# Optimization experiments

Measured on AMD Instinct MI355X. Metric: run time of the kernel, lower is better.

Reference implementation:

```python
import jax, jax.numpy as jnp
import numpy as np

N, E, F, H, EF, ED, L, NL, NH, OD = 2048, 65536, 128, 512, 16, 64, 5, 4, 8, 64
MAX_DEG = 64


def _ln(x, s, b):
    m = x.mean(-1, keepdims=True)
    v = x.var(-1, keepdims=True)
    return (x - m) * jax.lax.rsqrt(v + 1e-5) * s + b


def setup_inputs() -> dict:
    key = jax.random.key(0)
    ks = jax.random.split(key, 40)
    s = 0.02
    x = jax.random.normal(ks[0], (N, F), jnp.float32)
    edge_index = jax.random.randint(ks[1], (2, E), 0, N, jnp.int32)
    edge_attr = jax.random.normal(ks[2], (E, EF), jnp.float32)
    # variable-length shortest paths, padded with -1
    plen = jax.random.randint(ks[3], (N, N), 0, L + 1, jnp.int32)
    pos = jnp.arange(L, dtype=jnp.int32)
    valid = pos[None, None, :] < plen[:, :, None]
    node_paths = jnp.where(valid, jax.random.randint(ks[4], (N, N, L), 0, N, jnp.int32), -1)
    edge_paths = jnp.where(valid, jax.random.randint(ks[5], (N, N, L), 0, E, jnp.int32), -1)
    p = {
        'x': x, 'edge_index': edge_index, 'edge_attr': edge_attr,
        'node_paths': node_paths, 'edge_paths': edge_paths,
        'W_node': s * jax.random.normal(ks[6], (F, H)), 'b_node': jnp.zeros((H,)),
        'W_edge': s * jax.random.normal(ks[7], (EF, ED)), 'b_edge': jnp.zeros((ED,)),
        'z_in': s * jax.random.normal(ks[8], (MAX_DEG, H)),
        'z_out': s * jax.random.normal(ks[9], (MAX_DEG, H)),
        'b_spatial': s * jax.random.normal(ks[10], (L,)),
        'edge_vector': s * jax.random.normal(ks[11], (L, ED)),
        'ln1_s': jnp.ones((NL, H)), 'ln1_b': jnp.zeros((NL, H)),
        'Wq': s * jax.random.normal(ks[12], (NL, H, H)), 'bq': jnp.zeros((NL, H)),
        'Wk': s * jax.random.normal(ks[13], (NL, H, H)), 'bk': jnp.zeros((NL, H)),
        'Wv': s * jax.random.normal(ks[14], (NL, H, H)), 'bv': jnp.zeros((NL, H)),
        'Wo': s * jax.random.normal(ks[15], (NL, H, H)), 'bo': jnp.zeros((NL, H)),
        'ln2_s': jnp.ones((NL, H)), 'ln2_b': jnp.zeros((NL, H)),
        'W1': s * jax.random.normal(ks[16], (NL, H, H)), 'b1': jnp.zeros((NL, H)),
        'W2': s * jax.random.normal(ks[17], (NL, H, H)), 'b2': jnp.zeros((NL, H)),
        'W_out': s * jax.random.normal(ks[18], (H, OD)), 'b_out': jnp.zeros((OD,)),
    }
    return p


def reference(x, edge_index, edge_attr, node_paths, edge_paths,
              W_node, b_node, W_edge, b_edge, z_in, z_out, b_spatial, edge_vector,
              ln1_s, ln1_b, Wq, bq, Wk, bk, Wv, bv, Wo, bo,
              ln2_s, ln2_b, W1, b1, W2, b2, W_out, b_out):
    n = x.shape[0]
    dk = H // NH
    h = x @ W_node + b_node  # [N,H]
    # centrality encoding: in/out degree -> learned embeddings, clamped
    in_deg = jnp.clip(jnp.zeros((n,), jnp.int32).at[edge_index[1]].add(1), 0, MAX_DEG - 1)
    out_deg = jnp.clip(jnp.zeros((n,), jnp.int32).at[edge_index[0]].add(1), 0, MAX_DEG - 1)
    h = h + z_in[in_deg] + z_out[out_deg]
    # edge encoding: mean over path of <edge_vector[k], edge_emb[path_k]>
    e_emb = edge_attr @ W_edge + b_edge           # [E,ED]
    w = e_emb @ edge_vector.T                     # [E,L] per-position dot products
    valid_e = edge_paths >= 0
    gath = w[jnp.clip(edge_paths, 0), jnp.arange(L)[None, None, :]]  # [N,N,L]
    cnt = valid_e.sum(-1).astype(h.dtype)
    c = jnp.where(cnt > 0, (gath * valid_e).sum(-1) / jnp.maximum(cnt, 1.0), 0.0)  # [N,N]
    # spatial encoding: learned scalar per path length
    plen = (node_paths >= 0).sum(-1)
    b_sp = jnp.where(plen > 0, b_spatial[jnp.clip(plen - 1, 0, L - 1)], 0.0)  # [N,N]
    bias = b_sp + c
    scale = 1.0 / jnp.sqrt(jnp.asarray(dk, h.dtype))
    for l in range(NL):
        y = _ln(h, ln1_s[l], ln1_b[l])
        q = (y @ Wq[l] + bq[l]).reshape(n, NH, dk)
        k = (y @ Wk[l] + bk[l]).reshape(n, NH, dk)
        v = (y @ Wv[l] + bv[l]).reshape(n, NH, dk)
        scores = jnp.einsum('ihd,jhd->hij', q, k) * scale + bias[None]
        attn = jax.nn.softmax(scores, axis=-1)
        o = jnp.einsum('hij,jhd->ihd', attn, v).reshape(n, H)
        h = h + o @ Wo[l] + bo[l]
        y2 = _ln(h, ln2_s[l], ln2_b[l])
        h = h + jax.nn.gelu(y2 @ W1[l] + b1[l]) @ W2[l] + b2[l]
    return h @ W_out + b_out
```

## Files before the change

### kernel.cpp

```cpp
#include <hip/hip_runtime.h>
#include <hip/hip_bf16.h>
#include <math.h>

#define N_NODES 2048
#define NEDGE   65536
#define FDIM    128
#define HDIM    512
#define EFD     16
#define EDD     64
#define LPATH   5
#define NLAYER  4
#define NHEAD   8
#define DK      64
#define ODIM    64
#define MAXDEG  64
#define PTOT    4194304

typedef __bf16 bf16;
typedef bf16 bf16x8 __attribute__((ext_vector_type(8)));
typedef bf16 bf16x4 __attribute__((ext_vector_type(4)));
typedef float f32x4 __attribute__((ext_vector_type(4)));
typedef unsigned short u16;
typedef u16 u16x4 __attribute__((ext_vector_type(4)));

__global__ __launch_bounds__(256) void k_edge_w(const float* __restrict__ ea, const float* __restrict__ We,
                                                const float* __restrict__ be, const float* __restrict__ ev,
                                                bf16* __restrict__ wT) {
    __shared__ float sM[80];
    __shared__ float sc[8];
    int t = threadIdx.x;
    if (t < 80) {
        int i = t / 5, j = t % 5;
        float acc = 0.f;
        for (int k = 0; k < EDD; ++k) acc += We[i * EDD + k] * ev[j * EDD + k];
        sM[t] = acc;
    } else if (t >= 128 && t < 128 + LPATH) {
        int j = t - 128;
        float acc = 0.f;
        for (int k = 0; k < EDD; ++k) acc += be[k] * ev[j * EDD + k];
        sc[j] = acc;
    }
    __syncthreads();
    int e = blockIdx.x * 256 + t;
    const float4* p = (const float4*)(ea + (size_t)e * EFD);
    float4 a0 = p[0], a1 = p[1], a2 = p[2], a3 = p[3];
    float a[16] = {a0.x, a0.y, a0.z, a0.w, a1.x, a1.y, a1.z, a1.w,
                   a2.x, a2.y, a2.z, a2.w, a3.x, a3.y, a3.z, a3.w};
    float out[LPATH];
#pragma unroll
    for (int j = 0; j < LPATH; ++j) out[j] = sc[j];
#pragma unroll
    for (int i = 0; i < 16; ++i)
#pragma unroll
        for (int j = 0; j < LPATH; ++j) out[j] += a[i] * sM[i * LPATH + j];
#pragma unroll
    for (int j = 0; j < LPATH; ++j) wT[(size_t)j * NEDGE + e] = (bf16)out[j];
}

__global__ __launch_bounds__(256) void k_deg(const int* __restrict__ ei, int* __restrict__ din, int* __restrict__ dout) {
    int e = blockIdx.x * 256 + threadIdx.x;
    if (e < NEDGE) {
        atomicAdd(&dout[ei[e]], 1);
        atomicAdd(&din[ei[NEDGE + e]], 1);
    }
}

__global__ __launch_bounds__(256) void k_pack(const int* __restrict__ ep, u16* __restrict__ idxp,
                                              unsigned char* __restrict__ maskp) {
    __shared__ int ints[5120];
    int t = threadIdx.x;
    size_t blk = blockIdx.x;
    const int4* src = (const int4*)(ep + blk * 5120);
#pragma unroll
    for (int u = 0; u < 5; ++u) *(int4*)&ints[(t + 256 * u) * 4] = src[t + 256 * u];
    __syncthreads();
    u16x4 out[LPATH];
    unsigned m[4] = {0, 0, 0, 0};
#pragma unroll
    for (int j = 0; j < 4; ++j) {
        int p = t * 4 + j;
#pragma unroll
        for (int l = 0; l < LPATH; ++l) {
            int v = ints[p * 5 + l];
            if (v >= 0) m[j] |= (1u << l);
            out[l][j] = (u16)v;
        }
    }
#pragma unroll
    for (int l = 0; l < LPATH; ++l)
        *(u16x4*)(idxp + (size_t)l * PTOT + blk * 1024 + t * 4) = out[l];
    *(unsigned*)(maskp + blk * 1024 + t * 4) = m[0] | (m[1] << 8) | (m[2] << 16) | (m[3] << 24);
}

__global__ __launch_bounds__(1024) void k_bias2(const u16* __restrict__ idxp, const unsigned char* __restrict__ maskp,
                                                const bf16* __restrict__ wT, const float* __restrict__ bsp,
                                                bf16* __restrict__ bias) {
    __shared__ bf16 wsl[NEDGE];
    int t = threadIdx.x;
    int base = blockIdx.x * 8192;
    unsigned char msk[8];
    float csum[8] = {};
#pragma unroll
    for (int r = 0; r < 8; ++r) msk[r] = maskp[base + r * 1024 + t];
    for (int l = 0; l < LPATH; ++l) {
        __syncthreads();
#pragma unroll
        for (int u = 0; u < 4; ++u) {
            int o = u * 16384 + t * 16;
            *(bf16x8*)&wsl[o]     = *(const bf16x8*)&wT[(size_t)l * NEDGE + o];
            *(bf16x8*)&wsl[o + 8] = *(const bf16x8*)&wT[(size_t)l * NEDGE + o + 8];
        }
        u16 ei[8];
#pragma unroll
        for (int r = 0; r < 8; ++r) ei[r] = idxp[(size_t)l * PTOT + base + r * 1024 + t];
        __syncthreads();
#pragma unroll
        for (int r = 0; r < 8; ++r) {
            float v = (float)wsl[ei[r]];
            csum[r] += ((msk[r] >> l) & 1) ? v : 0.f;
        }
    }
#pragma unroll
    for (int r = 0; r < 8; ++r) {
        int cnt = __popc((int)msk[r]);
        float b = cnt ? bsp[cnt - 1] + csum[r] / (float)cnt : 0.f;
        bias[base + r * 1024 + t] = (bf16)b;
    }
}

__global__ __launch_bounds__(256) void k_ln(const float* __restrict__ h, const float* __restrict__ sc,
                                            const float* __restrict__ bi, bf16* __restrict__ y) {
    int i = blockIdx.x, t = threadIdx.x;
    float v0 = h[(size_t)i * HDIM + t];
    float v1 = h[(size_t)i * HDIM + 256 + t];
    float s = v0 + v1, q = v0 * v0 + v1 * v1;
#pragma unroll
    for (int m = 1; m < 64; m <<= 1) { s += __shfl_xor(s, m); q += __shfl_xor(q, m); }
    __shared__ float ssum[4], sq[4];
    int wv = t >> 6;
    if ((t & 63) == 0) { ssum[wv] = s; sq[wv] = q; }
    __syncthreads();
    float S = ssum[0] + ssum[1] + ssum[2] + ssum[3];
    float Q = sq[0] + sq[1] + sq[2] + sq[3];
    float mean = S * (1.f / HDIM);
    float var = Q * (1.f / HDIM) - mean * mean;
    float r = rsqrtf(var + 1e-5f);
    y[(size_t)i * HDIM + t] = (bf16)((v0 - mean) * r * sc[t] + bi[t]);
    y[(size_t)i * HDIM + 256 + t] = (bf16)((v1 - mean) * r * sc[256 + t] + bi[256 + t]);
}

__global__ __launch_bounds__(256) void k_wprep(const float* __restrict__ Wq, const float* __restrict__ Wk,
                                               const float* __restrict__ Wv, const float* __restrict__ Wo,
                                               const float* __restrict__ W1, const float* __restrict__ W2,
                                               bf16* __restrict__ Wt) {
    __shared__ float Ls[64][68];
    int m = blockIdx.y;
    int lay = m / 6, type = m % 6;
    const float* src = type == 0 ? Wq : type == 1 ? Wk : type == 2 ? Wv : type == 3 ? Wo : type == 4 ? W1 : W2;
    src += (size_t)lay * (HDIM * HDIM);
    int q = blockIdx.x;
    int tk = q >> 3, tn = q & 7;
    int t = threadIdx.x;
    int rr = t >> 4, cc = t & 15;
#pragma unroll
    for (int u = 0; u < 4; ++u) {
        float4 v = *(const float4*)(src + (size_t)(tk * 64 + rr + 16 * u) * HDIM + tn * 64 + cc * 4);
        *(float4*)&Ls[rr + 16 * u][cc * 4] = v;
    }
    __syncthreads();
    int nl = t >> 2, kc = t & 3;
    bf16 tmp[16];
#pragma unroll
    for (int u = 0; u < 16; ++u) tmp[u] = (bf16)Ls[kc * 16 + u][nl];
    bf16* dst = Wt + (size_t)m * (HDIM * HDIM) + (size_t)(tn * 64 + nl) * HDIM + tk * 64 + kc * 16;
    *(bf16x8*)(dst) = *(bf16x8*)&tmp[0];
    *(bf16x8*)(dst + 8) = *(bf16x8*)&tmp[8];
}

__global__ __launch_bounds__(256) void k_wprepn(const float* __restrict__ Wn, bf16* __restrict__ WnT) {
    __shared__ float Ls[64][68];
    int b = blockIdx.x;
    int tk = b >> 3, tn = b & 7;
    int t = threadIdx.x, rr = t >> 4, cc = t & 15;
#pragma unroll
    for (int u = 0; u < 4; ++u) {
        float4 v = *(const float4*)(Wn + (size_t)(tk * 64 + rr + 16 * u) * HDIM + tn * 64 + cc * 4);
        *(float4*)&Ls[rr + 16 * u][cc * 4] = v;
    }
    __syncthreads();
    int nl = t >> 2, kc = t & 3;
    bf16 tmp[16];
#pragma unroll
    for (int u = 0; u < 16; ++u) tmp[u] = (bf16)Ls[kc * 16 + u][nl];
    bf16* dst = WnT + (size_t)(tn * 64 + nl) * FDIM + tk * 64 + kc * 16;
    *(bf16x8*)dst = *(bf16x8*)&tmp[0];
    *(bf16x8*)(dst + 8) = *(bf16x8*)&tmp[8];
}

__global__ __launch_bounds__(256) void k_nmm(const float* __restrict__ x, const bf16* __restrict__ Bt,
                                             const float* __restrict__ bn, const float* __restrict__ zin,
                                             const float* __restrict__ zout, const int* __restrict__ din,
                                             const int* __restrict__ dout, float* __restrict__ h) {
    __shared__ bf16 Bs[8192];
    int t = threadIdx.x, w = t >> 6, l = t & 63, lr = l & 15, lg = l >> 4;
    int j0 = blockIdx.x * 64, i0 = blockIdx.y * 64;
    const bf16* Bp = Bt + (size_t)j0 * FDIM;
#pragma unroll
    for (int rnd = 0; rnd < 4; ++rnd) {
        int tt = rnd * 256 + t;
        int ks = tt >> 8, qq = (tt >> 6) & 3, mm = (tt >> 2) & 15, gg = tt & 3;
        *(bf16x8*)(Bs + tt * 8) = *(const bf16x8*)(Bp + (size_t)(qq * 16 + mm) * FDIM + ks * 32 + gg * 8);
    }
    __syncthreads();
    const float* ap = x + (size_t)(i0 + w * 16 + lr) * FDIM + 8 * lg;
    f32x4 acc[4] = {};
#pragma unroll
    for (int ks = 0; ks < 4; ++ks) {
        float4 f0 = *(const float4*)(ap + ks * 32);
        float4 f1 = *(const float4*)(ap + ks * 32 + 4);
        bf16x8 a;
        a[0] = (bf16)f0.x; a[1] = (bf16)f0.y; a[2] = (bf16)f0.z; a[3] = (bf16)f0.w;
        a[4] = (bf16)f1.x; a[5] = (bf16)f1.y; a[6] = (bf16)f1.z; a[7] = (bf16)f1.w;
        const bf16* bb = Bs + ks * 2048 + lr * 32 + lg * 8;
#pragma unroll
        for (int sub = 0; sub < 4; ++sub)
            acc[sub] = __builtin_amdgcn_mfma_f32_16x16x32_bf16(a, *(const bf16x8*)(bb + sub * 512), acc[sub], 0, 0, 0);
    }
#pragma unroll
    for (int r = 0; r < 4; ++r) {
        int i = i0 + w * 16 + lg * 4 + r;
        int di = min(din[i], MAXDEG - 1), dz = min(dout[i], MAXDEG - 1);
#pragma unroll
        for (int sub = 0; sub < 4; ++sub) {
            int j = j0 + sub * 16 + lr;
            h[(size_t)i * HDIM + j] = acc[sub][r] + bn[j] + zin[(size_t)di * HDIM + j] + zout[(size_t)dz * HDIM + j];
        }
    }
}

__global__ __launch_bounds__(256) void k_qkv(const bf16* __restrict__ A, const bf16* __restrict__ Wt_l,
                                             const float* __restrict__ bq, const float* __restrict__ bk,
                                             const float* __restrict__ bv, bf16* __restrict__ qf,
                                             bf16* __restrict__ kf, bf16* __restrict__ vf) {
    __shared__ bf16 Bs[16384];
    int t = threadIdx.x, w = t >> 6, l = t & 63, lr = l & 15, lg = l >> 4;
    int j0 = blockIdx.x * 32, i0 = blockIdx.y * 64;
    int type = j0 >> 9, n0 = j0 & 511;
    const bf16* Bp = Wt_l + (size_t)type * (HDIM * HDIM) + (size_t)n0 * HDIM;
#pragma unroll
    for (int rnd = 0; rnd < 8; ++rnd) {
        int tt = rnd * 256 + t;
        int ks = tt >> 7, qq = (tt >> 6) & 1, mm = (tt >> 2) & 15, gg = tt & 3;
        bf16x8 v = *(const bf16x8*)(Bp + (size_t)(qq * 16 + mm) * HDIM + ks * 32 + gg * 8);
        *(bf16x8*)(Bs + tt * 8) = v;
    }
    __syncthreads();
    const bf16* ap = A + (size_t)(i0 + w * 16 + lr) * HDIM + 8 * lg;
    const float* bvec = (type == 0 ? bq : type == 1 ? bk : bv);
    f32x4 acc[2] = {};
#pragma unroll 4
    for (int ks = 0; ks < 16; ++ks) {
        bf16x8 a  = *(const bf16x8*)(ap + ks * 32);
        const bf16* bb = Bs + ks * 1024 + lr * 32 + lg * 8;
        bf16x8 b0 = *(const bf16x8*)(bb);
        bf16x8 b1 = *(const bf16x8*)(bb + 512);
        acc[0] = __builtin_amdgcn_mfma_f32_16x16x32_bf16(a, b0, acc[0], 0, 0, 0);
        acc[1] = __builtin_amdgcn_mfma_f32_16x16x32_bf16(a, b1, acc[1], 0, 0, 0);
    }
    int h = n0 >> 6;
    if (type < 2) {
        bf16* dst = (type == 0 ? qf : kf);
        int hf = (n0 & 32) >> 5;
        float sc = (type == 0 ? 0.125f : 1.0f);
#pragma unroll
        for (int sub = 0; sub < 2; ++sub) {
#pragma unroll
            for (int r = 0; r < 4; ++r) {
                int i = i0 + w * 16 + lg * 4 + r;
                float v = (acc[sub][r] + bvec[n0 + sub * 16 + lr]) * sc;
                int lgp = sub * 2 + (lr >> 3);
                size_t off = (((size_t)(h * 128 + (i >> 4)) * 2 + hf) << 9) + lgp * 128 + (lg * 4 + r) * 8 + (lr & 7);
                dst[off] = (bf16)v;
            }
        }
    } else {
#pragma unroll
        for (int sub = 0; sub < 2; ++sub) {
#pragma unroll
            for (int r = 0; r < 4; ++r) {
                int node = i0 + w * 16 + lg * 4 + r;
                int dd = (n0 & 63) + sub * 16 + lr;
                float v = acc[sub][r] + bvec[n0 + sub * 16 + lr];
                size_t off = (((size_t)(h * 4 + (dd >> 4)) * 64 + (node >> 5)) << 9)
                           + ((node >> 3) & 3) * 128 + (dd & 15) * 8 + (node & 7);
                vf[off] = (bf16)v;
            }
        }
    }
}

#define FL_RES   1
#define FL_GELU  2
#define FL_OUTF  4

__device__ inline float gelu_f(float x) {
    float x3 = x * x * x;
    float u = 0.7978845608028654f * (x + 0.044715f * x3);
    return 0.5f * x * (1.f + tanhf(u));
}

__global__ __launch_bounds__(1024) void k_mm(const bf16* __restrict__ A, const bf16* __restrict__ Bt,
                                             const float* __restrict__ bvec, const float* __restrict__ res,
                                             float* __restrict__ outF, bf16* __restrict__ outB, int flags) {
    __shared__ bf16 Bs[32768];
    __shared__ float Osh[4][16][68];
    int t = threadIdx.x, w = t >> 6, l = t & 63, lr = l & 15, lg = l >> 4;
    int ti = w & 3, s = w >> 2;
    int j0 = blockIdx.x * 64, i0 = blockIdx.y * 64;
    const bf16* Bp = Bt + (size_t)j0 * HDIM;
#pragma unroll
    for (int rnd = 0; rnd < 4; ++rnd) {
        int tt = rnd * 1024 + t;
        int ks = tt >> 8, qq = (tt >> 6) & 3, mm = (tt >> 2) & 15, gg = tt & 3;
        bf16x8 v = *(const bf16x8*)(Bp + (size_t)(qq * 16 + mm) * HDIM + ks * 32 + gg * 8);
        *(bf16x8*)(Bs + tt * 8) = v;
    }
    __syncthreads();
    const bf16* ap = A + (size_t)(i0 + ti * 16 + lr) * HDIM + 8 * lg;
    f32x4 acc[4] = {};
#pragma unroll
    for (int kk = 0; kk < 4; ++kk) {
        int ks = s * 4 + kk;
        bf16x8 a = *(const bf16x8*)(ap + ks * 32);
        const bf16* bb = Bs + ks * 2048 + lr * 32 + lg * 8;
#pragma unroll
        for (int sub = 0; sub < 4; ++sub) {
            bf16x8 b = *(const bf16x8*)(bb + sub * 512);
            acc[sub] = __builtin_amdgcn_mfma_f32_16x16x32_bf16(a, b, acc[sub], 0, 0, 0);
        }
    }
    if (s == 0) {
#pragma unroll
        for (int sub = 0; sub < 4; ++sub)
#pragma unroll
            for (int r = 0; r < 4; ++r) Osh[ti][lg * 4 + r][sub * 16 + lr] = acc[sub][r];
    }
    __syncthreads();
    if (s == 1) {
#pragma unroll
        for (int sub = 0; sub < 4; ++sub)
#pragma unroll
            for (int r = 0; r < 4; ++r) Osh[ti][lg * 4 + r][sub * 16 + lr] += acc[sub][r];
    }
    __syncthreads();
    if (s == 2) {
#pragma unroll
        for (int sub = 0; sub < 4; ++sub)
#pragma unroll
            for (int r = 0; r < 4; ++r) Osh[ti][lg * 4 + r][sub * 16 + lr] += acc[sub][r];
    }
    __syncthreads();
    if (s == 3) {
#pragma unroll
        for (int sub = 0; sub < 4; ++sub) {
#pragma unroll
            for (int r = 0; r < 4; ++r) {
                int i = i0 + ti * 16 + lg * 4 + r;
                int j = j0 + sub * 16 + lr;
                float v = Osh[ti][lg * 4 + r][sub * 16 + lr] + acc[sub][r] + bvec[j];
                if (flags & FL_RES) v += res[(size_t)i * HDIM + j];
                if (flags & FL_GELU) v = gelu_f(v);
                if (flags & FL_OUTF) outF[(size_t)i * HDIM + j] = v;
                else outB[(size_t)i * HDIM + j] = (bf16)v;
            }
        }
    }
}

__global__ __launch_bounds__(1024) void k_mmln(const float* __restrict__ h, const bf16* __restrict__ Bt,
                                               const float* __restrict__ lnS, const float* __restrict__ lnB,
                                               const float* __restrict__ bvec, bf16* __restrict__ outB) {
    __shared__ bf16 As[32768];
    __shared__ bf16 Bs[32768];
    __shared__ float Osh[4][16][68];
    __shared__ float sbuf[HDIM], bbuf[HDIM];
    int t = threadIdx.x, w = t >> 6, l = t & 63, lr = l & 15, lg = l >> 4;
    int ti = w & 3, s = w >> 2;
    int j0 = blockIdx.x * 64, i0 = blockIdx.y * 64;
    if (t < HDIM) sbuf[t] = lnS[t];
    else bbuf[t - HDIM] = lnB[t - HDIM];
    const bf16* Bp = Bt + (size_t)j0 * HDIM;
#pragma unroll
    for (int rnd = 0; rnd < 4; ++rnd) {
        int tt = rnd * 1024 + t;
        int ks = tt >> 8, qq = (tt >> 6) & 3, mm = (tt >> 2) & 15, gg = tt & 3;
        *(bf16x8*)(Bs + tt * 8) = *(const bf16x8*)(Bp + (size_t)(qq * 16 + mm) * HDIM + ks * 32 + gg * 8);
    }
    int row = t >> 4, ksc = t & 15;
    const float* hp = h + (size_t)(i0 + row) * HDIM + ksc * 32;
    float4 hv[8];
    float S = 0.f, Q = 0.f;
#pragma unroll
    for (int u = 0; u < 8; ++u) {
        hv[u] = *(const float4*)(hp + u * 4);
        S += hv[u].x + hv[u].y + hv[u].z + hv[u].w;
        Q += hv[u].x * hv[u].x + hv[u].y * hv[u].y + hv[u].z * hv[u].z + hv[u].w * hv[u].w;
    }
#pragma unroll
    for (int m = 1; m < 16; m <<= 1) { S += __shfl_xor(S, m); Q += __shfl_xor(Q, m); }
    float mean = S * (1.f / HDIM);
    float var = Q * (1.f / HDIM) - mean * mean;
    float rr = rsqrtf(var + 1e-5f);
    float ca = rr, cc = -mean * rr;
    __syncthreads();
    {
        bf16 tmp[32];
#pragma unroll
        for (int u = 0; u < 8; ++u) {
            float vv[4] = {hv[u].x, hv[u].y, hv[u].z, hv[u].w};
#pragma unroll
            for (int c = 0; c < 4; ++c) {
                int col = ksc * 32 + u * 4 + c;
                tmp[u * 4 + c] = (bf16)(fmaf(fmaf(vv[c], ca, cc), sbuf[col], bbuf[col]));
            }
        }
        bf16* dst = As + (row >> 4) * 8192 + ksc * 512 + (row & 15) * 32;
#pragma unroll
        for (int u = 0; u < 4; ++u) *(bf16x8*)(dst + u * 8) = *(bf16x8*)&tmp[u * 8];
    }
    __syncthreads();
    const bf16* apl = As + ti * 8192 + lr * 32 + lg * 8;
    f32x4 acc[4] = {};
#pragma unroll
    for (int kk = 0; kk < 4; ++kk) {
        int ks = s * 4 + kk;
        bf16x8 a = *(const bf16x8*)(apl + ks * 512);
        const bf16* bb = Bs + ks * 2048 + lr * 32 + lg * 8;
#pragma unroll
        for (int sub = 0; sub < 4; ++sub)
            acc[sub] = __builtin_amdgcn_mfma_f32_16x16x32_bf16(a, *(const bf16x8*)(bb + sub * 512), acc[sub], 0, 0, 0);
    }
    if (s == 0) {
#pragma unroll
        for (int sub = 0; sub < 4; ++sub)
#pragma unroll
            for (int r = 0; r < 4; ++r) Osh[ti][lg * 4 + r][sub * 16 + lr] = acc[sub][r];
    }
    __syncthreads();
    if (s == 1) {
#pragma unroll
        for (int sub = 0; sub < 4; ++sub)
#pragma unroll
            for (int r = 0; r < 4; ++r) Osh[ti][lg * 4 + r][sub * 16 + lr] += acc[sub][r];
    }
    __syncthreads();
    if (s == 2) {
#pragma unroll
        for (int sub = 0; sub < 4; ++sub)
#pragma unroll
            for (int r = 0; r < 4; ++r) Osh[ti][lg * 4 + r][sub * 16 + lr] += acc[sub][r];
    }
    __syncthreads();
    if (s == 3) {
#pragma unroll
        for (int sub = 0; sub < 4; ++sub) {
#pragma unroll
            for (int r = 0; r < 4; ++r) {
                int i = i0 + ti * 16 + lg * 4 + r;
                int j = j0 + sub * 16 + lr;
                float v = gelu_f(Osh[ti][lg * 4 + r][sub * 16 + lr] + acc[sub][r] + bvec[j]);
                outB[(size_t)i * HDIM + j] = (bf16)v;
            }
        }
    }
}

__global__ __launch_bounds__(1024) void k_attn2(const bf16* __restrict__ qf, const bf16* __restrict__ kf,
                                                const bf16* __restrict__ vf, const bf16* __restrict__ biasb,
                                                bf16* __restrict__ ob) {
    __shared__ char Pb[16 * 1024];
    __shared__ float Osh[4][64][17];
    __shared__ float Msh[4][4][16], Lsh[4][4][16];
    int t = threadIdx.x, w = t >> 6, l = t & 63, lr = l & 15, lg = l >> 4;
    int ti = w & 3, s = w >> 2;
    int bid = blockIdx.x;
    int wid = (bid & 7) * 32 + (bid >> 3);
    int i0 = (wid >> 3) * 64, hh = wid & 7;
    int irow = i0 + ti * 16;

    const bf16* qb = qf + (((size_t)(hh * 128 + (irow >> 4)) * 2) << 9) + l * 8;
    bf16x8 qy0 = *(const bf16x8*)(qb);
    bf16x8 qy1 = *(const bf16x8*)(qb + 512);

    char* pwr = Pb + w * 1024 + lr * 64;
    unsigned kx = (unsigned)(lr & 6) << 3;

    float m_run = -3e38f, l_run = 0.f;
    f32x4 oacc[4] = {};

    for (int it = 0; it < 16; ++it) {
        int jb = s * 512 + it * 32;
        const bf16* kb = kf + (((size_t)(hh * 128 + (jb >> 4)) * 2) << 9) + l * 8;
        bf16x8 kx00 = *(const bf16x8*)(kb);
        bf16x8 kx01 = *(const bf16x8*)(kb + 512);
        bf16x8 kx10 = *(const bf16x8*)(kb + 1024);
        bf16x8 kx11 = *(const bf16x8*)(kb + 1536);
        const bf16* vb = vf + (((size_t)(hh * 4) * 64 + (jb >> 5)) << 9) + l * 8;
        bf16x8 vx0 = *(const bf16x8*)(vb);
        bf16x8 vx1 = *(const bf16x8*)(vb + 32768);
        bf16x8 vx2 = *(const bf16x8*)(vb + 65536);
        bf16x8 vx3 = *(const bf16x8*)(vb + 98304);
        const bf16* bp = biasb + (size_t)(irow + lr) * N_NODES + jb + lg * 4;
        bf16x4 bv0 = *(const bf16x4*)(bp);
        bf16x4 bv1 = *(const bf16x4*)(bp + 16);

        f32x4 s0v = {}, s1v = {};
        __builtin_amdgcn_s_setprio(1);
        s0v = __builtin_amdgcn_mfma_f32_16x16x32_bf16(kx00, qy0, s0v, 0, 0, 0);
        s0v = __builtin_amdgcn_mfma_f32_16x16x32_bf16(kx01, qy1, s0v, 0, 0, 0);
        s1v = __builtin_amdgcn_mfma_f32_16x16x32_bf16(kx10, qy0, s1v, 0, 0, 0);
        s1v = __builtin_amdgcn_mfma_f32_16x16x32_bf16(kx11, qy1, s1v, 0, 0, 0);
        __builtin_amdgcn_s_setprio(0);

        float p0[4], p1[4];
        float mt = -3e38f;
#pragma unroll
        for (int r = 0; r < 4; ++r) {
            p0[r] = s0v[r] + (float)bv0[r];
            p1[r] = s1v[r] + (float)bv1[r];
            mt = fmaxf(mt, fmaxf(p0[r], p1[r]));
        }
        mt = fmaxf(mt, __shfl_xor(mt, 16));
        mt = fmaxf(mt, __shfl_xor(mt, 32));
        if (!__all(mt <= m_run + 8.f)) {
            float mn = fmaxf(m_run, mt);
            float alpha = __expf(m_run - mn);
            l_run *= alpha;
#pragma unroll
            for (int d = 0; d < 4; ++d) oacc[d] *= alpha;
            m_run = mn;
        }
        float ps = 0.f;
        bf16x4 pk0, pk1;
#pragma unroll
        for (int r = 0; r < 4; ++r) {
            p0[r] = __expf(p0[r] - m_run);
            p1[r] = __expf(p1[r] - m_run);
            ps += p0[r] + p1[r];
            pk0[r] = (bf16)p0[r];
            pk1[r] = (bf16)p1[r];
        }
        ps += __shfl_xor(ps, 16);
        ps += __shfl_xor(ps, 32);
        l_run += ps;

        *(bf16x4*)(pwr + ((lg * 8) ^ kx)) = pk0;
        *(bf16x4*)(pwr + ((32 + lg * 8) ^ kx)) = pk1;
        asm volatile("s_waitcnt lgkmcnt(0)" ::: "memory");
        __builtin_amdgcn_sched_barrier(0x20);
        bf16x8 py = *(bf16x8*)(Pb + w * 1024 + lr * 64 + ((lg * 16) ^ kx));
        __builtin_amdgcn_s_setprio(1);
        oacc[0] = __builtin_amdgcn_mfma_f32_16x16x32_bf16(vx0, py, oacc[0], 0, 0, 0);
        oacc[1] = __builtin_amdgcn_mfma_f32_16x16x32_bf16(vx1, py, oacc[1], 0, 0, 0);
        oacc[2] = __builtin_amdgcn_mfma_f32_16x16x32_bf16(vx2, py, oacc[2], 0, 0, 0);
        oacc[3] = __builtin_amdgcn_mfma_f32_16x16x32_bf16(vx3, py, oacc[3], 0, 0, 0);
        __builtin_amdgcn_s_setprio(0);
    }

    __syncthreads();
    if (lg == 0) { Msh[ti][s][lr] = m_run; Lsh[ti][s][lr] = l_run; }
    __syncthreads();
    float m0 = Msh[ti][0][lr], m1 = Msh[ti][1][lr], m2 = Msh[ti][2][lr], m3 = Msh[ti][3][lr];
    float mtot = fmaxf(fmaxf(m0, m1), fmaxf(m2, m3));
    float l_tot = Lsh[ti][0][lr] * __expf(m0 - mtot) + Lsh[ti][1][lr] * __expf(m1 - mtot)
                + Lsh[ti][2][lr] * __expf(m2 - mtot) + Lsh[ti][3][lr] * __expf(m3 - mtot);
    float fac = __expf(m_run - mtot);
#pragma unroll
    for (int d = 0; d < 4; ++d) oacc[d] *= fac;
    if (s == 0) {
#pragma unroll
        for (int db = 0; db < 4; ++db)
#pragma unroll
            for (int r = 0; r < 4; ++r) Osh[ti][db * 16 + lg * 4 + r][lr] = oacc[db][r];
    }
    __syncthreads();
    if (s == 1) {
#pragma unroll
        for (int db = 0; db < 4; ++db)
#pragma unroll
            for (int r = 0; r < 4; ++r) Osh[ti][db * 16 + lg * 4 + r][lr] += oacc[db][r];
    }
    __syncthreads();
    if (s == 2) {
#pragma unroll
        for (int db = 0; db < 4; ++db)
#pragma unroll
            for (int r = 0; r < 4; ++r) Osh[ti][db * 16 + lg * 4 + r][lr] += oacc[db][r];
    }
    __syncthreads();
    if (s == 3) {
        float inv = 1.f / l_tot;
#pragma unroll
        for (int db = 0; db < 4; ++db) {
            bf16x4 o4;
#pragma unroll
            for (int r = 0; r < 4; ++r)
                o4[r] = (bf16)((Osh[ti][db * 16 + lg * 4 + r][lr] + oacc[db][r]) * inv);
            *(bf16x4*)(ob + (size_t)(irow + lr) * HDIM + hh * DK + db * 16 + lg * 4) = o4;
        }
    }
}

__global__ __launch_bounds__(256) void k_gemm(const float* __restrict__ A, const float* __restrict__ B,
                                              const float* __restrict__ bvec, float* __restrict__ C,
                                              int M, int Nc, int K) {
    __shared__ float As[16][68];
    __shared__ float Bs[16][68];
    int t = threadIdx.x;
    int tm = t >> 4, tn = t & 15;
    int i0 = blockIdx.y * 64, j0 = blockIdx.x * 64;
    int ar = t >> 2, aq = t & 3;
    int br = t >> 4, bq = t & 15;
    float acc[4][4] = {};
    for (int k0 = 0; k0 < K; k0 += 16) {
        float4 av = *(const float4*)(A + (size_t)(i0 + ar) * K + k0 + aq * 4);
        As[aq * 4 + 0][ar] = av.x;
        As[aq * 4 + 1][ar] = av.y;
        As[aq * 4 + 2][ar] = av.z;
        As[aq * 4 + 3][ar] = av.w;
        *(float4*)&Bs[br][bq * 4] = *(const float4*)(B + (size_t)(k0 + br) * Nc + j0 + bq * 4);
        __syncthreads();
#pragma unroll
        for (int k = 0; k < 16; ++k) {
            float4 a4 = *(const float4*)&As[k][tm * 4];
            float4 b4 = *(const float4*)&Bs[k][tn * 4];
            float avv[4] = {a4.x, a4.y, a4.z, a4.w};
            float bvv[4] = {b4.x, b4.y, b4.z, b4.w};
#pragma unroll
            for (int r = 0; r < 4; ++r)
#pragma unroll
                for (int c = 0; c < 4; ++c) acc[r][c] += avv[r] * bvv[c];
        }
        __syncthreads();
    }
#pragma unroll
    for (int r = 0; r < 4; ++r) {
#pragma unroll
        for (int c = 0; c < 4; ++c) {
            int i = i0 + tm * 4 + r;
            int j = j0 + tn * 4 + c;
            C[(size_t)i * Nc + j] = acc[r][c] + bvec[j];
        }
    }
}

extern "C" void kernel_launch(void* const* d_in, const int* in_sizes, int n_in,
                              void* d_out, int out_size, void* d_ws, size_t ws_size,
                              hipStream_t stream) {
    const float* x      = (const float*)d_in[0];
    const int*   ei     = (const int*)d_in[1];
    const float* eattr  = (const float*)d_in[2];
    const int*   epaths = (const int*)d_in[4];
    const float* Wn     = (const float*)d_in[5];
    const float* bn     = (const float*)d_in[6];
    const float* We     = (const float*)d_in[7];
    const float* be     = (const float*)d_in[8];
    const float* zin    = (const float*)d_in[9];
    const float* zout   = (const float*)d_in[10];
    const float* bsp    = (const float*)d_in[11];
    const float* ev     = (const float*)d_in[12];
    const float* ln1s   = (const float*)d_in[13];
    const float* ln1b   = (const float*)d_in[14];
    const float* Wq     = (const float*)d_in[15];
    const float* bq     = (const float*)d_in[16];
    const float* Wk     = (const float*)d_in[17];
    const float* bk     = (const float*)d_in[18];
    const float* Wv     = (const float*)d_in[19];
    const float* bv     = (const float*)d_in[20];
    const float* Wo     = (const float*)d_in[21];
    const float* bo     = (const float*)d_in[22];
    const float* ln2s   = (const float*)d_in[23];
    const float* ln2b   = (const float*)d_in[24];
    const float* W1     = (const float*)d_in[25];
    const float* b1     = (const float*)d_in[26];
    const float* W2     = (const float*)d_in[27];
    const float* b2     = (const float*)d_in[28];
    const float* Wout   = (const float*)d_in[29];
    const float* bout   = (const float*)d_in[30];

    char* base = (char*)d_ws;
    size_t off = 0;
    auto alloc = [&](size_t bytes) { char* p = base + off; off = (off + bytes + 255) & ~(size_t)255; return p; };
    bf16*  bias   = (bf16*)alloc((size_t)N_NODES * N_NODES * 2);
    float* h      = (float*)alloc((size_t)N_NODES * HDIM * 4);
    bf16*  wT     = (bf16*)alloc((size_t)LPATH * NEDGE * 2);
    int*   deg    = (int*)alloc(2 * N_NODES * 4);
    u16*   idxp   = (u16*)alloc((size_t)LPATH * PTOT * 2);
    unsigned char* maskp = (unsigned char*)alloc((size_t)PTOT);
    bf16*  WnT    = (bf16*)alloc((size_t)HDIM * FDIM * 2);
    bf16*  Wt     = (bf16*)alloc((size_t)NLAYER * 6 * HDIM * HDIM * 2);
    bf16*  y_bf   = (bf16*)alloc((size_t)N_NODES * HDIM * 2);
    bf16*  qfb    = (bf16*)alloc((size_t)NHEAD * 128 * 2 * 512 * 2);
    bf16*  kfb    = (bf16*)alloc((size_t)NHEAD * 128 * 2 * 512 * 2);
    bf16*  vfb    = (bf16*)alloc((size_t)NHEAD * 4 * 64 * 512 * 2);
    bf16*  ob_bf  = (bf16*)alloc((size_t)N_NODES * HDIM * 2);
    bf16*  t1_bf  = (bf16*)alloc((size_t)N_NODES * HDIM * 2);
    int* din = deg;
    int* dout = deg + N_NODES;

    hipMemsetAsync(deg, 0, 2 * N_NODES * sizeof(int), stream);

    k_edge_w<<<NEDGE / 256, 256, 0, stream>>>(eattr, We, be, ev, wT);
    k_deg<<<NEDGE / 256, 256, 0, stream>>>(ei, din, dout);
    k_pack<<<PTOT / 1024, 256, 0, stream>>>(epaths, idxp, maskp);
    k_bias2<<<512, 1024, 0, stream>>>(idxp, maskp, wT, bsp, bias);
    k_wprep<<<dim3(64, 24), 256, 0, stream>>>(Wq, Wk, Wv, Wo, W1, W2, Wt);
    k_wprepn<<<16, 256, 0, stream>>>(Wn, WnT);
    k_nmm<<<dim3(8, 32), 256, 0, stream>>>(x, WnT, bn, zin, zout, din, dout, h);

    dim3 gqkv(48, 32);
    dim3 gmm(8, 32);

    for (int lay = 0; lay < NLAYER; ++lay) {
        const bf16* Wt_l = Wt + (size_t)lay * 6 * HDIM * HDIM;
        size_t bOff = (size_t)lay * HDIM;
        k_ln<<<N_NODES, 256, 0, stream>>>(h, ln1s + bOff, ln1b + bOff, y_bf);
        k_qkv<<<gqkv, 256, 0, stream>>>(y_bf, Wt_l, bq + bOff, bk + bOff, bv + bOff, qfb, kfb, vfb);
        k_attn2<<<256, 1024, 0, stream>>>(qfb, kfb, vfb, bias, ob_bf);
        k_mm<<<gmm, 1024, 0, stream>>>(ob_bf, Wt_l + (size_t)3 * HDIM * HDIM, bo + bOff, h, h, nullptr, FL_RES | FL_OUTF);
        k_mmln<<<gmm, 1024, 0, stream>>>(h, Wt_l + (size_t)4 * HDIM * HDIM, ln2s + bOff, ln2b + bOff, b1 + bOff, t1_bf);
        k_mm<<<gmm, 1024, 0, stream>>>(t1_bf, Wt_l + (size_t)5 * HDIM * HDIM, b2 + bOff, h, h, nullptr, FL_RES | FL_OUTF);
    }
    k_gemm<<<dim3(1, 32), 256, 0, stream>>>(h, Wout, bout, (float*)d_out, N_NODES, ODIM, HDIM);
}
```

Measured before the change: 506.5 us.

## Fuse preprocessing kernels and prefetch K/bias in attention loop

Folds the degree-count atomics into the edge-weight kernel, merges the path-packing and bias-gather kernels into one kernel that packs indices in LDS and registers, and merges the node-weight transpose into the layer-weight prep kernel. This drops several launches and the intermediate idxp/mask round trip through global memory, about 50MB of writes and reads. The attention inner loop now loads the next iteration's K fragments and bias values one step ahead so their latency overlaps the current MFMA and softmax work. In exchange it uses more registers in attention, and the fused bias kernel needs 160KB of LDS per block.

```diff
diff --git a/kernel.cpp b/kernel.cpp
--- a/kernel.cpp
+++ b/kernel.cpp
@@ -21,11 +21,11 @@
 typedef bf16 bf16x4 __attribute__((ext_vector_type(4)));
 typedef float f32x4 __attribute__((ext_vector_type(4)));
 typedef unsigned short u16;
-typedef u16 u16x4 __attribute__((ext_vector_type(4)));
 
 __global__ __launch_bounds__(256) void k_edge_w(const float* __restrict__ ea, const float* __restrict__ We,
                                                 const float* __restrict__ be, const float* __restrict__ ev,
-                                                bf16* __restrict__ wT) {
+                                                const int* __restrict__ ei, int* __restrict__ din,
+                                                int* __restrict__ dout, bf16* __restrict__ wT) {
     __shared__ float sM[80];
     __shared__ float sc[8];
     int t = threadIdx.x;
@@ -40,8 +40,10 @@
         for (int k = 0; k < EDD; ++k) acc += be[k] * ev[j * EDD + k];
         sc[j] = acc;
     }
-    __syncthreads();
     int e = blockIdx.x * 256 + t;
+    atomicAdd(&dout[ei[e]], 1);
+    atomicAdd(&din[ei[NEDGE + e]], 1);
+    __syncthreads();
     const float4* p = (const float4*)(ea + (size_t)e * EFD);
     float4 a0 = p[0], a1 = p[1], a2 = p[2], a3 = p[3];
     float a[16] = {a0.x, a0.y, a0.z, a0.w, a1.x, a1.y, a1.z, a1.w,
@@ -57,51 +59,30 @@
     for (int j = 0; j < LPATH; ++j) wT[(size_t)j * NEDGE + e] = (bf16)out[j];
 }
 
-__global__ __launch_bounds__(256) void k_deg(const int* __restrict__ ei, int* __restrict__ din, int* __restrict__ dout) {
-    int e = blockIdx.x * 256 + threadIdx.x;
-    if (e < NEDGE) {
-        atomicAdd(&dout[ei[e]], 1);
-        atomicAdd(&din[ei[NEDGE + e]], 1);
-    }
-}
-
-__global__ __launch_bounds__(256) void k_pack(const int* __restrict__ ep, u16* __restrict__ idxp,
-                                              unsigned char* __restrict__ maskp) {
-    __shared__ int ints[5120];
+__global__ __launch_bounds__(1024) void k_bias3(const int* __restrict__ ep, const bf16* __restrict__ wT,
+                                                const float* __restrict__ bsp, bf16* __restrict__ bias) {
+    __shared__ char lds[163840];
     int t = threadIdx.x;
-    size_t blk = blockIdx.x;
-    const int4* src = (const int4*)(ep + blk * 5120);
-#pragma unroll
-    for (int u = 0; u < 5; ++u) *(int4*)&ints[(t + 256 * u) * 4] = src[t + 256 * u];
-    __syncthreads();
-    u16x4 out[LPATH];
-    unsigned m[4] = {0, 0, 0, 0};
-#pragma unroll
-    for (int j = 0; j < 4; ++j) {
-        int p = t * 4 + j;
-#pragma unroll
-        for (int l = 0; l < LPATH; ++l) {
-            int v = ints[p * 5 + l];
-            if (v >= 0) m[j] |= (1u << l);
-            out[l][j] = (u16)v;
-        }
-    }
-#pragma unroll
-    for (int l = 0; l < LPATH; ++l)
-        *(u16x4*)(idxp + (size_t)l * PTOT + blk * 1024 + t * 4) = out[l];
-    *(unsigned*)(maskp + blk * 1024 + t * 4) = m[0] | (m[1] << 8) | (m[2] << 16) | (m[3] << 24);
-}
-
-__global__ __launch_bounds__(1024) void k_bias2(const u16* __restrict__ idxp, const unsigned char* __restrict__ maskp,
-                                                const bf16* __restrict__ wT, const float* __restrict__ bsp,
-                                                bf16* __restrict__ bias) {
-    __shared__ bf16 wsl[NEDGE];
-    int t = threadIdx.x;
-    int base = blockIdx.x * 8192;
-    unsigned char msk[8];
+    size_t basep = (size_t)blockIdx.x * 8192;
+    int* ish = (int*)lds;
+    const int4* src = (const int4*)(ep + basep * 5);
+#pragma unroll
+    for (int u = 0; u < 10; ++u) ((int4*)ish)[t + 1024 * u] = src[t + 1024 * u];
+    __syncthreads();
+    unsigned pa[8], pb[8], pc[8];
+#pragma unroll
+    for (int r = 0; r < 8; ++r) {
+        int p5 = (r * 1024 + t) * 5;
+        int e0 = ish[p5], e1 = ish[p5 + 1], e2 = ish[p5 + 2], e3 = ish[p5 + 3], e4 = ish[p5 + 4];
+        unsigned mk = (unsigned)(e0 >= 0) | ((unsigned)(e1 >= 0) << 1) | ((unsigned)(e2 >= 0) << 2)
+                    | ((unsigned)(e3 >= 0) << 3) | ((unsigned)(e4 >= 0) << 4);
+        pa[r] = ((unsigned)e0 & 0xFFFFu) | ((unsigned)e1 << 16);
+        pb[r] = ((unsigned)e2 & 0xFFFFu) | ((unsigned)e3 << 16);
+        pc[r] = ((unsigned)e4 & 0xFFFFu) | (mk << 16);
+    }
+    bf16* wsl = (bf16*)lds;
     float csum[8] = {};
 #pragma unroll
-    for (int r = 0; r < 8; ++r) msk[r] = maskp[base + r * 1024 + t];
     for (int l = 0; l < LPATH; ++l) {
         __syncthreads();
 #pragma unroll
@@ -110,21 +91,20 @@
             *(bf16x8*)&wsl[o]     = *(const bf16x8*)&wT[(size_t)l * NEDGE + o];
             *(bf16x8*)&wsl[o + 8] = *(const bf16x8*)&wT[(size_t)l * NEDGE + o + 8];
         }
-        u16 ei[8];
-#pragma unroll
-        for (int r = 0; r < 8; ++r) ei[r] = idxp[(size_t)l * PTOT + base + r * 1024 + t];
         __syncthreads();
 #pragma unroll
         for (int r = 0; r < 8; ++r) {
-            float v = (float)wsl[ei[r]];
-            csum[r] += ((msk[r] >> l) & 1) ? v : 0.f;
+            unsigned ix = (l == 0) ? (pa[r] & 0xFFFFu) : (l == 1) ? (pa[r] >> 16)
+                        : (l == 2) ? (pb[r] & 0xFFFFu) : (l == 3) ? (pb[r] >> 16) : (pc[r] & 0xFFFFu);
+            float v = (float)wsl[ix];
+            csum[r] += ((pc[r] >> (16 + l)) & 1u) ? v : 0.f;
         }
     }
 #pragma unroll
     for (int r = 0; r < 8; ++r) {
-        int cnt = __popc((int)msk[r]);
+        int cnt = __popc((int)((pc[r] >> 16) & 0x1Fu));
         float b = cnt ? bsp[cnt - 1] + csum[r] / (float)cnt : 0.f;
-        bias[base + r * 1024 + t] = (bf16)b;
+        bias[basep + r * 1024 + t] = (bf16)b;
     }
 }
 
@@ -152,49 +132,47 @@
 __global__ __launch_bounds__(256) void k_wprep(const float* __restrict__ Wq, const float* __restrict__ Wk,
                                                const float* __restrict__ Wv, const float* __restrict__ Wo,
                                                const float* __restrict__ W1, const float* __restrict__ W2,
-                                               bf16* __restrict__ Wt) {
+                                               const float* __restrict__ Wn, bf16* __restrict__ Wt,
+                                               bf16* __restrict__ WnT) {
     __shared__ float Ls[64][68];
     int m = blockIdx.y;
-    int lay = m / 6, type = m % 6;
-    const float* src = type == 0 ? Wq : type == 1 ? Wk : type == 2 ? Wv : type == 3 ? Wo : type == 4 ? W1 : W2;
-    src += (size_t)lay * (HDIM * HDIM);
     int q = blockIdx.x;
-    int tk = q >> 3, tn = q & 7;
     int t = threadIdx.x;
     int rr = t >> 4, cc = t & 15;
-#pragma unroll
-    for (int u = 0; u < 4; ++u) {
-        float4 v = *(const float4*)(src + (size_t)(tk * 64 + rr + 16 * u) * HDIM + tn * 64 + cc * 4);
-        *(float4*)&Ls[rr + 16 * u][cc * 4] = v;
-    }
-    __syncthreads();
     int nl = t >> 2, kc = t & 3;
-    bf16 tmp[16];
-#pragma unroll
-    for (int u = 0; u < 16; ++u) tmp[u] = (bf16)Ls[kc * 16 + u][nl];
-    bf16* dst = Wt + (size_t)m * (HDIM * HDIM) + (size_t)(tn * 64 + nl) * HDIM + tk * 64 + kc * 16;
-    *(bf16x8*)(dst) = *(bf16x8*)&tmp[0];
-    *(bf16x8*)(dst + 8) = *(bf16x8*)&tmp[8];
-}
-
-__global__ __launch_bounds__(256) void k_wprepn(const float* __restrict__ Wn, bf16* __restrict__ WnT) {
-    __shared__ float Ls[64][68];
-    int b = blockIdx.x;
-    int tk = b >> 3, tn = b & 7;
-    int t = threadIdx.x, rr = t >> 4, cc = t & 15;
-#pragma unroll
-    for (int u = 0; u < 4; ++u) {
-        float4 v = *(const float4*)(Wn + (size_t)(tk * 64 + rr + 16 * u) * HDIM + tn * 64 + cc * 4);
-        *(float4*)&Ls[rr + 16 * u][cc * 4] = v;
-    }
-    __syncthreads();
-    int nl = t >> 2, kc = t & 3;
-    bf16 tmp[16];
-#pragma unroll
-    for (int u = 0; u < 16; ++u) tmp[u] = (bf16)Ls[kc * 16 + u][nl];
-    bf16* dst = WnT + (size_t)(tn * 64 + nl) * FDIM + tk * 64 + kc * 16;
-    *(bf16x8*)dst = *(bf16x8*)&tmp[0];
-    *(bf16x8*)(dst + 8) = *(bf16x8*)&tmp[8];
+    if (m < 24) {
+        int lay = m / 6, type = m % 6;
+        const float* src = type == 0 ? Wq : type == 1 ? Wk : type == 2 ? Wv : type == 3 ? Wo : type == 4 ? W1 : W2;
+        src += (size_t)lay * (HDIM * HDIM);
+        int tk = q >> 3, tn = q & 7;
+#pragma unroll
+        for (int u = 0; u < 4; ++u) {
+            float4 v = *(const float4*)(src + (size_t)(tk * 64 + rr + 16 * u) * HDIM + tn * 64 + cc * 4);
+            *(float4*)&Ls[rr + 16 * u][cc * 4] = v;
+        }
+        __syncthreads();
+        bf16 tmp[16];
+#pragma unroll
+        for (int u = 0; u < 16; ++u) tmp[u] = (bf16)Ls[kc * 16 + u][nl];
+        bf16* dst = Wt + (size_t)m * (HDIM * HDIM) + (size_t)(tn * 64 + nl) * HDIM + tk * 64 + kc * 16;
+        *(bf16x8*)(dst) = *(bf16x8*)&tmp[0];
+        *(bf16x8*)(dst + 8) = *(bf16x8*)&tmp[8];
+    } else {
+        if (q >= 16) return;
+        int tk = q >> 3, tn = q & 7;
+#pragma unroll
+        for (int u = 0; u < 4; ++u) {
+            float4 v = *(const float4*)(Wn + (size_t)(tk * 64 + rr + 16 * u) * HDIM + tn * 64 + cc * 4);
+            *(float4*)&Ls[rr + 16 * u][cc * 4] = v;
+        }
+        __syncthreads();
+        bf16 tmp[16];
+#pragma unroll
+        for (int u = 0; u < 16; ++u) tmp[u] = (bf16)Ls[kc * 16 + u][nl];
+        bf16* dst = WnT + (size_t)(tn * 64 + nl) * FDIM + tk * 64 + kc * 16;
+        *(bf16x8*)dst = *(bf16x8*)&tmp[0];
+        *(bf16x8*)(dst + 8) = *(bf16x8*)&tmp[8];
+    }
 }
 
 __global__ __launch_bounds__(256) void k_nmm(const float* __restrict__ x, const bf16* __restrict__ Bt,
@@ -498,36 +476,51 @@
     float m_run = -3e38f, l_run = 0.f;
     f32x4 oacc[4] = {};
 
+    int jb0 = s * 512;
+    const bf16* kbp = kf + (((size_t)(hh * 128 + (jb0 >> 4)) * 2) << 9) + l * 8;
+    bf16x8 ka0 = *(const bf16x8*)(kbp);
+    bf16x8 ka1 = *(const bf16x8*)(kbp + 512);
+    bf16x8 ka2 = *(const bf16x8*)(kbp + 1024);
+    bf16x8 ka3 = *(const bf16x8*)(kbp + 1536);
+    const bf16* bpp = biasb + (size_t)(irow + lr) * N_NODES + jb0 + lg * 4;
+    bf16x4 ba0 = *(const bf16x4*)(bpp);
+    bf16x4 ba1 = *(const bf16x4*)(bpp + 16);
+
     for (int it = 0; it < 16; ++it) {
         int jb = s * 512 + it * 32;
-        const bf16* kb = kf + (((size_t)(hh * 128 + (jb >> 4)) * 2) << 9) + l * 8;
-        bf16x8 kx00 = *(const bf16x8*)(kb);
-        bf16x8 kx01 = *(const bf16x8*)(kb + 512);
-        bf16x8 kx10 = *(const bf16x8*)(kb + 1024);
-        bf16x8 kx11 = *(const bf16x8*)(kb + 1536);
         const bf16* vb = vf + (((size_t)(hh * 4) * 64 + (jb >> 5)) << 9) + l * 8;
         bf16x8 vx0 = *(const bf16x8*)(vb);
         bf16x8 vx1 = *(const bf16x8*)(vb + 32768);
         bf16x8 vx2 = *(const bf16x8*)(vb + 65536);
         bf16x8 vx3 = *(const bf16x8*)(vb + 98304);
-        const bf16* bp = biasb + (size_t)(irow + lr) * N_NODES + jb + lg * 4;
-        bf16x4 bv0 = *(const bf16x4*)(bp);
-        bf16x4 bv1 = *(const bf16x4*)(bp + 16);
+        bf16x8 kn0, kn1, kn2, kn3;
+        bf16x4 bn0, bn1;
+        if (it < 15) {
+            int jn = jb + 32;
+            const bf16* kbn = kf + (((size_t)(hh * 128 + (jn >> 4)) * 2) << 9) + l * 8;
+            kn0 = *(const bf16x8*)(kbn);
+            kn1 = *(const bf16x8*)(kbn + 512);
+            kn2 = *(const bf16x8*)(kbn + 1024);
+            kn3 = *(const bf16x8*)(kbn + 1536);
+            const bf16* bpn = biasb + (size_t)(irow + lr) * N_NODES + jn + lg * 4;
+            bn0 = *(const bf16x4*)(bpn);
+            bn1 = *(const bf16x4*)(bpn + 16);
+        }
 
         f32x4 s0v = {}, s1v = {};
         __builtin_amdgcn_s_setprio(1);
-        s0v = __builtin_amdgcn_mfma_f32_16x16x32_bf16(kx00, qy0, s0v, 0, 0, 0);
-        s0v = __builtin_amdgcn_mfma_f32_16x16x32_bf16(kx01, qy1, s0v, 0, 0, 0);
-        s1v = __builtin_amdgcn_mfma_f32_16x16x32_bf16(kx10, qy0, s1v, 0, 0, 0);
-        s1v = __builtin_amdgcn_mfma_f32_16x16x32_bf16(kx11, qy1, s1v, 0, 0, 0);
+        s0v = __builtin_amdgcn_mfma_f32_16x16x32_bf16(ka0, qy0, s0v, 0, 0, 0);
+        s0v = __builtin_amdgcn_mfma_f32_16x16x32_bf16(ka1, qy1, s0v, 0, 0, 0);
+        s1v = __builtin_amdgcn_mfma_f32_16x16x32_bf16(ka2, qy0, s1v, 0, 0, 0);
+        s1v = __builtin_amdgcn_mfma_f32_16x16x32_bf16(ka3, qy1, s1v, 0, 0, 0);
         __builtin_amdgcn_s_setprio(0);
 
         float p0[4], p1[4];
         float mt = -3e38f;
 #pragma unroll
         for (int r = 0; r < 4; ++r) {
-            p0[r] = s0v[r] + (float)bv0[r];
-            p1[r] = s1v[r] + (float)bv1[r];
+            p0[r] = s0v[r] + (float)ba0[r];
+            p1[r] = s1v[r] + (float)ba1[r];
             mt = fmaxf(mt, fmaxf(p0[r], p1[r]));
         }
         mt = fmaxf(mt, __shfl_xor(mt, 16));
@@ -565,6 +558,8 @@
         oacc[2] = __builtin_amdgcn_mfma_f32_16x16x32_bf16(vx2, py, oacc[2], 0, 0, 0);
         oacc[3] = __builtin_amdgcn_mfma_f32_16x16x32_bf16(vx3, py, oacc[3], 0, 0, 0);
         __builtin_amdgcn_s_setprio(0);
+        ka0 = kn0; ka1 = kn1; ka2 = kn2; ka3 = kn3;
+        ba0 = bn0; ba1 = bn1;
     }
 
     __syncthreads();
@@ -695,8 +690,6 @@
     float* h      = (float*)alloc((size_t)N_NODES * HDIM * 4);
     bf16*  wT     = (bf16*)alloc((size_t)LPATH * NEDGE * 2);
     int*   deg    = (int*)alloc(2 * N_NODES * 4);
-    u16*   idxp   = (u16*)alloc((size_t)LPATH * PTOT * 2);
-    unsigned char* maskp = (unsigned char*)alloc((size_t)PTOT);
     bf16*  WnT    = (bf16*)alloc((size_t)HDIM * FDIM * 2);
     bf16*  Wt     = (bf16*)alloc((size_t)NLAYER * 6 * HDIM * HDIM * 2);
     bf16*  y_bf   = (bf16*)alloc((size_t)N_NODES * HDIM * 2);
@@ -710,12 +703,9 @@
 
     hipMemsetAsync(deg, 0, 2 * N_NODES * sizeof(int), stream);
 
-    k_edge_w<<<NEDGE / 256, 256, 0, stream>>>(eattr, We, be, ev, wT);
-    k_deg<<<NEDGE / 256, 256, 0, stream>>>(ei, din, dout);
-    k_pack<<<PTOT / 1024, 256, 0, stream>>>(epaths, idxp, maskp);
-    k_bias2<<<512, 1024, 0, stream>>>(idxp, maskp, wT, bsp, bias);
-    k_wprep<<<dim3(64, 24), 256, 0, stream>>>(Wq, Wk, Wv, Wo, W1, W2, Wt);
-    k_wprepn<<<16, 256, 0, stream>>>(Wn, WnT);
+    k_edge_w<<<NEDGE / 256, 256, 0, stream>>>(eattr, We, be, ev, ei, din, dout, wT);
+    k_bias3<<<512, 1024, 0, stream>>>(epaths, wT, bsp, bias);
+    k_wprep<<<dim3(64, 25), 256, 0, stream>>>(Wq, Wk, Wv, Wo, W1, W2, Wn, Wt, WnT);
     k_nmm<<<dim3(8, 32), 256, 0, stream>>>(x, WnT, bn, zin, zout, din, dout, h);
 
     dim3 gqkv(48, 32);
```

Result: faster. 481.2 us (-5.0%).
